# Optimization experiments

Measured on AMD Instinct MI355X. Metric: run time of the kernel, lower is better.

Reference implementation:

```python
import jax, jax.numpy as jnp
import numpy as np
from jax.scipy.linalg import solve_triangular

B, M, S, NBPS = 32768, 16, 8, 4
NUM_ITER = 2
EPS = 1e-4

def _pam_gray(b):
    if len(b) > 1:
        return (1 - 2 * b[0]) * (2 ** len(b[1:]) - _pam_gray(b[1:]))
    return 1 - 2 * b[0]

def _qam(nbps):
    n = 2 ** nbps
    pts = np.zeros(n, np.complex64)
    for i in range(n):
        b = np.array([int(c) for c in np.binary_repr(i, nbps)])
        pts[i] = _pam_gray(b[0::2]) + 1j * _pam_gray(b[1::2])
    pts = pts / np.sqrt(np.mean(np.abs(pts) ** 2))
    labels = ((np.arange(n)[:, None] >> np.arange(nbps - 1, -1, -1)) & 1).astype(np.float32)
    return pts.astype(np.complex64), labels

_PTS_NP, _LAB_NP = _qam(NBPS)
PTS = jnp.asarray(_PTS_NP)                                   # [P] complex64, unit-energy Gray QAM16
PTS_E = jnp.asarray((np.abs(_PTS_NP) ** 2).astype(np.float32))  # [P]
LAB = jnp.asarray(_LAB_NP)                                   # [P, K] bit labels (MSB first)
ASGN = 2.0 * LAB - 1.0                                       # [P, K], +1 where bit==1

def _symbol_logits(llr):
    # LLRs2SymbolLogits: llr=[...,S,K] (llr = log p(b=1)/p(b=0)) -> per-point log-prior [...,S,P]
    return jnp.sum(jax.nn.log_sigmoid(ASGN * llr[..., None, :]), axis=-1)

def _moments(logits):
    # SymbolLogits2Moments: softmax over points -> mean / variance of soft symbols
    p = jax.nn.softmax(logits, axis=-1)                       # [..., S, P]
    mean = jnp.einsum('...p,p->...', p.astype(jnp.complex64), PTS)
    e2 = jnp.einsum('...p,p->...', p, PTS_E)
    var = e2 - (mean.real ** 2 + mean.imag ** 2)
    return mean, var

def _demap(x_hat, llr_a, no_eff):
    # maxlog DemapperWithPrior, LLR = log p(b=1)/p(b=0)
    diff = x_hat[..., None] - PTS                             # [..., S, P]
    d2 = diff.real ** 2 + diff.imag ** 2
    exps = -d2 / no_eff[..., None] + _symbol_logits(llr_a)    # [..., S, P]
    e = exps[..., None]                                       # [..., S, P, 1]
    neg = jnp.float32(-1e30)
    l1 = jnp.max(jnp.where(LAB == 1.0, e, neg), axis=-2)      # [..., S, K]
    l0 = jnp.max(jnp.where(LAB == 0.0, e, neg), axis=-2)
    return l1 - l0

def _forward(y_re, y_im, h_re, h_im, prior, s_re, s_im):
    y = jax.lax.complex(y_re, y_im)                           # [B, M]
    h = jax.lax.complex(h_re, h_im)                           # [B, M, S]
    s = jax.lax.complex(s_re, s_im)                           # [B, M, M] Hermitian PSD
    # whiten_channel: s = L L^H, y <- L^-1 y, h <- L^-1 h
    L = jnp.linalg.cholesky(s)
    y = solve_triangular(L, y[..., None], lower=True)[..., 0]
    h = solve_triangular(L, h, lower=True)
    y_mf = jnp.einsum('bms,bm->bs', jnp.conj(h), y)[..., None]   # [B, S, 1] matched filter
    g = jnp.einsum('bmi,bmj->bij', jnp.conj(h), h)               # [B, S, S] Gram matrix
    # real-valued channel representation [[Re,-Im],[Im,Re]]
    hr = jnp.concatenate([
        jnp.concatenate([h.real, -h.imag], axis=-1),
        jnp.concatenate([h.imag, h.real], axis=-1)], axis=-2)    # [B, 2M, 2S]
    gr = jnp.einsum('bmi,bmj->bij', hr, hr)                      # [B, 2S, 2S]
    eye2s = jnp.eye(2 * S, dtype=jnp.float32)
    llr_d = prior
    llr_a = jnp.zeros_like(prior)
    for _ in range(NUM_ITER):
        llr_a = llr_d
        x_hat, var_x = _moments(_symbol_logits(llr_a))           # [B, S]
        # parallel interference cancellation in matched-filter domain
        y_mf_pic = (y_mf + g * x_hat[..., None, :]
                    - jnp.einsum('bij,bj->bi', g, x_hat)[..., None])  # [B, S, S]
        var2 = jnp.concatenate([var_x, var_x], axis=-1)          # [B, 2S]
        a = gr * var2[..., None, :] + eye2s                      # [B, 2S, 2S]
        a_inv = jnp.linalg.inv(a)
        mu = jnp.sum(a_inv * jnp.swapaxes(gr, -1, -2), axis=-1)  # diag(a_inv @ gr), [B, 2S]
        ypt = jnp.swapaxes(y_mf_pic, -1, -2)                     # [B, S, S] (stream-major)
        ypt_r = jnp.concatenate([ypt.real, ypt.imag], axis=-1)   # [B, S, 2S]
        ypt_r = jnp.concatenate([ypt_r, ypt_r], axis=-2)         # [B, 2S, 2S]
        z = jnp.sum(a_inv * ypt_r, axis=-1) / mu                 # [B, 2S] unbiased estimates
        zr, zi = jnp.split(z, 2, axis=-1)
        x_hat = jax.lax.complex(zr, zi)                          # [B, S]
        rho = mu / jnp.maximum(1.0 - var2 * mu, EPS)             # post-equalization SINR
        rho = jnp.split(rho, 2, axis=-1)[0]                      # [B, S]
        no_eff = 1.0 / rho
        llr_d = _demap(x_hat, llr_a, no_eff)
    return llr_d - llr_a  # extrinsic LLRs [B, S, K]

def setup_inputs() -> dict:
    key = jax.random.key(0)
    k = jax.random.split(key, 7)
    y_re = jax.random.normal(k[0], (B, M), jnp.float32)
    y_im = jax.random.normal(k[1], (B, M), jnp.float32)
    h_re = jax.random.normal(k[2], (B, M, S), jnp.float32) / np.float32(np.sqrt(2.0))
    h_im = jax.random.normal(k[3], (B, M, S), jnp.float32) / np.float32(np.sqrt(2.0))
    prior = 0.5 * jax.random.normal(k[4], (B, S, NBPS), jnp.float32)
    a = jax.lax.complex(jax.random.normal(k[5], (B, M, M), jnp.float32),
                        jax.random.normal(k[6], (B, M, M), jnp.float32)) / np.float32(np.sqrt(2.0 * M))
    s = jnp.einsum('bij,bkj->bik', a, jnp.conj(a)) + 0.5 * jnp.eye(M, dtype=jnp.complex64)
    return {"y_re": y_re, "y_im": y_im, "h_re": h_re, "h_im": h_im,
            "prior": prior, "s_re": s.real, "s_im": s.imag}

def reference(y_re, y_im, h_re, h_im, prior, s_re, s_im):
    return _forward(y_re, y_im, h_re, h_im, prior, s_re, s_im)
```

## Files before the change

### kernel.cpp

```cpp
#include <hip/hip_runtime.h>


#define EPS_F 1e-4f
#define INV_SQRT10 0.31622776601683794f
#define WSYNC() __builtin_amdgcn_wave_barrier()

__device__ __forceinline__ float rcpf(float x) { return __builtin_amdgcn_rcpf(x); }
__device__ __forceinline__ float rsqf(float x) { return __builtin_amdgcn_rsqf(x); }
__device__ __forceinline__ float rdlane(float v, int l) {
    return __uint_as_float(__builtin_amdgcn_readlane(__float_as_uint(v), l));
}
template<int OFF>
__device__ __forceinline__ float swzf(float v) {
    return __uint_as_float(__builtin_amdgcn_ds_swizzle(__float_as_uint(v), OFF));
}
#define SWX1 0x041F
#define SWX2 0x081F
#define SWX4 0x101F

__device__ __forceinline__ float pt_re(int p) {
    return (1.0f - 2.0f * (float)((p >> 3) & 1)) * (1.0f + 2.0f * (float)((p >> 1) & 1)) * INV_SQRT10;
}
__device__ __forceinline__ float pt_im(int p) {
    return (1.0f - 2.0f * (float)((p >> 2) & 1)) * (1.0f + 2.0f * (float)(p & 1)) * INV_SQRT10;
}

__global__ __launch_bounds__(256, 4)
void mmse_pic_kernel(const float* __restrict__ y_re, const float* __restrict__ y_im,
                     const float* __restrict__ h_re, const float* __restrict__ h_im,
                     const float* __restrict__ prior,
                     const float* __restrict__ s_re, const float* __restrict__ s_im,
                     float* __restrict__ out)
{
    const int lane = threadIdx.x & 63;
    const int w    = threadIdx.x >> 6;
    const int b    = blockIdx.x * 4 + w;
    const size_t bs = (size_t)b;

    __shared__ __align__(16) float2 Sc[4][16][28];
    __shared__ float2 xc_[4][8];
    __shared__ float2 ymc_[4][8];
    __shared__ float  vx_[4][8], ne_[4][8];
    __shared__ float  lsig[4][64];
    __shared__ float  logit_[4][8][20];
    __shared__ float  llrD_[4][8][4];

    {
        const float4* pr4 = (const float4*)(s_re + bs * 256);
        const float4* pi4 = (const float4*)(s_im + bs * 256);
        float4 vr = pr4[lane], vi = pi4[lane];
        int r = lane >> 2, c0 = (lane & 3) << 2;
        Sc[w][r][c0+0] = make_float2(vr.x, vi.x);
        Sc[w][r][c0+1] = make_float2(vr.y, vi.y);
        Sc[w][r][c0+2] = make_float2(vr.z, vi.z);
        Sc[w][r][c0+3] = make_float2(vr.w, vi.w);
        if (lane < 32) {
            const float4* hr4 = (const float4*)(h_re + bs * 128);
            const float4* hi4 = (const float4*)(h_im + bs * 128);
            float4 hr = hr4[lane], hi = hi4[lane];
            int row = lane >> 1, col = 16 + ((lane & 1) << 2);
            Sc[w][row][col+0] = make_float2(hr.x, hi.x);
            Sc[w][row][col+1] = make_float2(hr.y, hi.y);
            Sc[w][row][col+2] = make_float2(hr.z, hi.z);
            Sc[w][row][col+3] = make_float2(hr.w, hi.w);
        }
        if (lane < 16) Sc[w][lane][24] = make_float2(y_re[bs*16+lane], y_im[bs*16+lane]);
        if (lane < 32) ((float*)llrD_[w])[lane] = prior[bs*32 + lane];
    }
    WSYNC();

    {
        const int cj = min((lane & 15) << 1, 26);
        const int r4 = lane >> 4;
        float4* rowp[4];
        #pragma unroll
        for (int p = 0; p < 4; ++p)
            rowp[p] = (float4*)&Sc[w][(p << 2) + r4][cj];
        float4* pivp = (float4*)&Sc[w][0][cj];
        #pragma unroll
        for (int k = 0; k < 15; ++k) {
            float invd = rcpf(Sc[w][k][k].x);
            float4 rk = pivp[k * 14];
            const int pmin = (k + 1) >> 2;
            #pragma unroll
            for (int p = 0; p < 4; ++p) {
                if (p < pmin) continue;
                int i = (p << 2) + r4;
                float2 aik = Sc[w][i][k];
                float mr = aik.x * invd, mi = aik.y * invd;
                if (i <= k) { mr = 0.f; mi = 0.f; }
                float4 a = rowp[p][0];
                a.x -= mr*rk.x - mi*rk.y;
                a.y -= mr*rk.y + mi*rk.x;
                a.z -= mr*rk.z - mi*rk.w;
                a.w -= mr*rk.w + mi*rk.z;
                rowp[p][0] = a;
            }
            WSYNC();
        }
    }
    {
        int r2 = lane >> 2, c = lane & 3;
        float irs = rsqf(Sc[w][r2][r2].x);
        float2 v0 = Sc[w][r2][16 + c];
        Sc[w][r2][16 + c] = make_float2(v0.x*irs, v0.y*irs);
        float2 v1 = Sc[w][r2][20 + c];
        Sc[w][r2][20 + c] = make_float2(v1.x*irs, v1.y*irs);
        if (c == 0) {
            float2 v2 = Sc[w][r2][24];
            Sc[w][r2][24] = make_float2(v2.x*irs, v2.y*irs);
        }
    }
    WSYNC();

    const int s = lane >> 3, u = lane & 7;
    float g_re = 0.f, g_im = 0.f, ym_r = 0.f, ym_i = 0.f;
    #pragma unroll
    for (int m = 0; m < 16; ++m) {
        float2 a  = Sc[w][m][16 + s];
        float2 x  = Sc[w][m][16 + u];
        float2 xy = Sc[w][m][24];
        g_re += a.x*x.x + a.y*x.y;
        g_im += a.x*x.y - a.y*x.x;
        ym_r += a.x*xy.x + a.y*xy.y;
        ym_i += a.x*xy.y - a.y*xy.x;
    }
    if (u == 0) ymc_[w][s] = make_float2(ym_r, ym_i);
    WSYNC();

    const float pr = pt_re(u), pi2 = pt_im(u), pe = pr*pr + pi2*pi2;
    float llr_a_reg = 0.f;

    for (int it = 0; it < 2; ++it) {
        {
            int ts = lane >> 3, tk = (lane >> 1) & 3, sg = lane & 1;
            float v = llrD_[w][ts][tk];
            float x = sg ? v : -v;
            lsig[w][lane] = fminf(x, 0.f) - __logf(1.0f + __expf(-fabsf(x)));
        }
        if (lane < 32) llr_a_reg = ((float*)llrD_[w])[lane];
        WSYNC();
        int base = s << 3;
        float lc = lsig[w][base | 2 | ((u >> 2) & 1)]
                 + lsig[w][base | 4 | ((u >> 1) & 1)]
                 + lsig[w][base | 6 | (u & 1)];
        float l0 = lc + lsig[w][base];
        float l1 = lc + lsig[w][base | 1];
        {
            float mx = fmaxf(l0, l1);
            mx = fmaxf(mx, swzf<SWX1>(mx));
            mx = fmaxf(mx, swzf<SWX2>(mx));
            mx = fmaxf(mx, swzf<SWX4>(mx));
            float w0 = __expf(l0 - mx), w1 = __expf(l1 - mx);
            float a = w0 + w1, dw = w0 - w1;
            float se = a, mr = dw * pr, mi = a * pi2, e2 = a * pe;
            se += swzf<SWX1>(se); mr += swzf<SWX1>(mr); mi += swzf<SWX1>(mi); e2 += swzf<SWX1>(e2);
            se += swzf<SWX2>(se); mr += swzf<SWX2>(mr); mi += swzf<SWX2>(mi); e2 += swzf<SWX2>(e2);
            se += swzf<SWX4>(se); mr += swzf<SWX4>(mr); mi += swzf<SWX4>(mi); e2 += swzf<SWX4>(e2);
            if (u == 0) {
                float inv = rcpf(se);
                float mxr = mr*inv, mxi = mi*inv;
                xc_[w][s] = make_float2(mxr, mxi);
                vx_[w][s] = e2*inv - (mxr*mxr + mxi*mxi);
            }
        }
        WSYNC();
        float2 xj = xc_[w][u];
        float vj = vx_[w][u];
        float tr = g_re*xj.x - g_im*xj.y;
        float ti = g_re*xj.y + g_im*xj.x;
        tr += swzf<SWX1>(tr); ti += swzf<SWX1>(ti);
        tr += swzf<SWX2>(tr); ti += swzf<SWX2>(ti);
        tr += swzf<SWX4>(tr); ti += swzf<SWX4>(ti);
        float2 ym = ymc_[w][s];
        float br_ = ym.x - tr, bi_ = ym.y - ti;
        float Ar = g_re*vj + ((s == u) ? 1.f : 0.f);
        float Ai = g_im*vj;
        float Cr = g_re, Ci = g_im;
        #define GJ_STEP(K) { \
            float pvr = rdlane(Ar, (K)*9), pvi = rdlane(Ai, (K)*9); \
            int rowsrc = ((K)<<3)|u; \
            float rAr = __shfl(Ar, rowsrc), rAi = __shfl(Ai, rowsrc); \
            float rCr = __shfl(Cr, rowsrc), rCi = __shfl(Ci, rowsrc); \
            float rbr = __shfl(br_, rowsrc), rbi = __shfl(bi_, rowsrc); \
            float cAr = swzf<(((K)<<5)|0x18)>(Ar), cAi = swzf<(((K)<<5)|0x18)>(Ai); \
            float id2 = rcpf(pvr*pvr + pvi*pvi); \
            float ipr2 = pvr*id2, ipi2 = -pvi*id2; \
            float mr2 = cAr*ipr2 - cAi*ipi2; \
            float mi2 = cAr*ipi2 + cAi*ipr2; \
            if (s == (K)) { mr2 = 0.f; mi2 = 0.f; } \
            Ar  -= mr2*rAr - mi2*rAi;  Ai  -= mr2*rAi + mi2*rAr; \
            Cr  -= mr2*rCr - mi2*rCi;  Ci  -= mr2*rCi + mi2*rCr; \
            br_ -= mr2*rbr - mi2*rbi;  bi_ -= mr2*rbi + mi2*rbr; }
        GJ_STEP(0) GJ_STEP(1) GJ_STEP(2) GJ_STEP(3)
        GJ_STEP(4) GJ_STEP(5) GJ_STEP(6) GJ_STEP(7)
        #undef GJ_STEP
        if (s == u) {
            float id3 = rcpf(Ar*Ar + Ai*Ai);
            float ipr3 = Ar*id3, ipi3 = -Ai*id3;
            float wr = br_*ipr3 - bi_*ipi3;
            float wi = br_*ipi3 + bi_*ipr3;
            float ccr = Cr*ipr3 - Ci*ipi3;
            float cci = Cr*ipi3 + Ci*ipr3;
            float mu = ccr;
            float im = rcpf(mu);
            float zr = (wr + ccr*xj.x - cci*xj.y) * im;
            float zi = (wi + ccr*xj.y + cci*xj.x) * im;
            xc_[w][s] = make_float2(zr, zi);
            ne_[w][s] = fmaxf(1.f - vx_[w][s]*mu, EPS_F) * im;
        }
        WSYNC();
        {
            float2 xh = xc_[w][s];
            float idn = rcpf(ne_[w][s]);
            float dr0 = xh.x - pr, dr1 = xh.x + pr, di = xh.y - pi2;
            logit_[w][s][u]     = l0 - (dr0*dr0 + di*di) * idn;
            logit_[w][s][u + 8] = l1 - (dr1*dr1 + di*di) * idn;
        }
        WSYNC();
        {
            int s2 = lane >> 3, kb = (lane >> 1) & 3, half = lane & 1;
            int bitpos = 3 - kb;
            float m = -1e30f;
            #pragma unroll
            for (int q = 0; q < 8; ++q) {
                int low  = q & ((1 << bitpos) - 1);
                int high = (q >> bitpos) << (bitpos + 1);
                int p = high | (half << bitpos) | low;
                m = fmaxf(m, logit_[w][s2][p]);
            }
            float other = swzf<SWX1>(m);
            if (half == 1) llrD_[w][s2][kb] = m - other;
        }
        WSYNC();
    }

    if (lane < 32) out[bs*32 + lane] = ((float*)llrD_[w])[lane] - llr_a_reg;
}

extern "C" void kernel_launch(void* const* d_in, const int* in_sizes, int n_in,
                              void* d_out, int out_size, void* d_ws, size_t ws_size,
                              hipStream_t stream) {
    const float* y_re  = (const float*)d_in[0];
    const float* y_im  = (const float*)d_in[1];
    const float* h_re  = (const float*)d_in[2];
    const float* h_im  = (const float*)d_in[3];
    const float* prior = (const float*)d_in[4];
    const float* s_re  = (const float*)d_in[5];
    const float* s_im  = (const float*)d_in[6];
    float* out = (float*)d_out;

    const int B = in_sizes[0] / 16;
    mmse_pic_kernel<<<dim3(B / 4), dim3(256), 0, stream>>>(
        y_re, y_im, h_re, h_im, prior, s_re, s_im, out);
}
```

Baseline: 237.5 us.

## Process two batch elements per wavefront with interleaved independent phases

Each wavefront now handles two batch elements (A and B), interleaving their load, Cholesky-style elimination, Gram, moment, Gauss-Jordan solve and demap phases so that independent instruction streams can hide latency of LDS, shuffles and transcendental ops. The grid is halved and shared memory doubled. The elimination step is also rewritten from float4 column chunks to per-lane float2 columns limited to the active region (j>k). This raises register and LDS use per block, which may reduce occupancy under the launch bound of 4 blocks.

```diff
diff --git a/kernel.cpp b/kernel.cpp
--- a/kernel.cpp
+++ b/kernel.cpp
@@ -34,208 +34,247 @@
 {
     const int lane = threadIdx.x & 63;
     const int w    = threadIdx.x >> 6;
-    const int b    = blockIdx.x * 4 + w;
-    const size_t bs = (size_t)b;
-
-    __shared__ __align__(16) float2 Sc[4][16][28];
-    __shared__ float2 xc_[4][8];
-    __shared__ float2 ymc_[4][8];
-    __shared__ float  vx_[4][8], ne_[4][8];
-    __shared__ float  lsig[4][64];
-    __shared__ float  logit_[4][8][20];
-    __shared__ float  llrD_[4][8][4];
+    const int slA  = w << 1, slB = slA | 1;
+    const size_t bsA = (size_t)(blockIdx.x * 8 + slA);
+    const size_t bsB = bsA + 1;
+
+    __shared__ float2 Sc[8][16][28];
+    __shared__ float2 xc_[8][8];
+    __shared__ float2 ymc_[8][8];
+    __shared__ float  vx_[8][8], ne_[8][8];
+    __shared__ float  lsig[8][64];
+    __shared__ float  logit_[8][8][20];
+    __shared__ float  llrD_[8][8][4];
+
+#define LOADPH(X) { \
+        const float4* pr4 = (const float4*)(s_re + bs##X * 256); \
+        const float4* pi4 = (const float4*)(s_im + bs##X * 256); \
+        float4 vr = pr4[lane], vi = pi4[lane]; \
+        int r = lane >> 2, c0 = (lane & 3) << 2; \
+        Sc[sl##X][r][c0+0] = make_float2(vr.x, vi.x); \
+        Sc[sl##X][r][c0+1] = make_float2(vr.y, vi.y); \
+        Sc[sl##X][r][c0+2] = make_float2(vr.z, vi.z); \
+        Sc[sl##X][r][c0+3] = make_float2(vr.w, vi.w); \
+        if (lane < 32) { \
+            const float4* hr4 = (const float4*)(h_re + bs##X * 128); \
+            const float4* hi4 = (const float4*)(h_im + bs##X * 128); \
+            float4 hr = hr4[lane], hi = hi4[lane]; \
+            int row = lane >> 1, col = 16 + ((lane & 1) << 2); \
+            Sc[sl##X][row][col+0] = make_float2(hr.x, hi.x); \
+            Sc[sl##X][row][col+1] = make_float2(hr.y, hi.y); \
+            Sc[sl##X][row][col+2] = make_float2(hr.z, hi.z); \
+            Sc[sl##X][row][col+3] = make_float2(hr.w, hi.w); \
+        } \
+        if (lane < 16) Sc[sl##X][lane][24] = make_float2(y_re[bs##X*16+lane], y_im[bs##X*16+lane]); \
+        if (lane < 32) ((float*)llrD_[sl##X])[lane] = prior[bs##X*32 + lane]; \
+    }
+    LOADPH(A) LOADPH(B)
+#undef LOADPH
+    WSYNC();
 
     {
-        const float4* pr4 = (const float4*)(s_re + bs * 256);
-        const float4* pi4 = (const float4*)(s_im + bs * 256);
-        float4 vr = pr4[lane], vi = pi4[lane];
-        int r = lane >> 2, c0 = (lane & 3) << 2;
-        Sc[w][r][c0+0] = make_float2(vr.x, vi.x);
-        Sc[w][r][c0+1] = make_float2(vr.y, vi.y);
-        Sc[w][r][c0+2] = make_float2(vr.z, vi.z);
-        Sc[w][r][c0+3] = make_float2(vr.w, vi.w);
-        if (lane < 32) {
-            const float4* hr4 = (const float4*)(h_re + bs * 128);
-            const float4* hi4 = (const float4*)(h_im + bs * 128);
-            float4 hr = hr4[lane], hi = hi4[lane];
-            int row = lane >> 1, col = 16 + ((lane & 1) << 2);
-            Sc[w][row][col+0] = make_float2(hr.x, hi.x);
-            Sc[w][row][col+1] = make_float2(hr.y, hi.y);
-            Sc[w][row][col+2] = make_float2(hr.z, hi.z);
-            Sc[w][row][col+3] = make_float2(hr.w, hi.w);
-        }
-        if (lane < 16) Sc[w][lane][24] = make_float2(y_re[bs*16+lane], y_im[bs*16+lane]);
-        if (lane < 32) ((float*)llrD_[w])[lane] = prior[bs*32 + lane];
-    }
-    WSYNC();
-
-    {
-        const int cj = min((lane & 15) << 1, 26);
+        const int j0 = lane & 15;
         const int r4 = lane >> 4;
-        float4* rowp[4];
-        #pragma unroll
-        for (int p = 0; p < 4; ++p)
-            rowp[p] = (float4*)&Sc[w][(p << 2) + r4][cj];
-        float4* pivp = (float4*)&Sc[w][0][cj];
+#define ELIMSTEP(X) { \
+            float invd = rcpf(Sc[sl##X][k][k].x); \
+            int j1 = k + 1 + j0, j2 = j1 + 16; \
+            float2 rk0 = make_float2(0.f, 0.f), rk1 = make_float2(0.f, 0.f); \
+            if (j1 < 25) rk0 = Sc[sl##X][k][j1]; \
+            const bool blk2 = (k < 8); \
+            if (blk2 && j2 < 25) rk1 = Sc[sl##X][k][j2]; \
+            const int pmin = (k + 1) >> 2; \
+            _Pragma("unroll") \
+            for (int p = 0; p < 4; ++p) { \
+                if (p < pmin) continue; \
+                int i = (p << 2) + r4; \
+                float2 aik = Sc[sl##X][i][k]; \
+                float mr = aik.x * invd, mi = aik.y * invd; \
+                if (i <= k) { mr = 0.f; mi = 0.f; } \
+                if (j1 < 25) { \
+                    float2 a = Sc[sl##X][i][j1]; \
+                    a.x -= mr*rk0.x - mi*rk0.y; \
+                    a.y -= mr*rk0.y + mi*rk0.x; \
+                    Sc[sl##X][i][j1] = a; \
+                } \
+                if (blk2 && j2 < 25) { \
+                    float2 a = Sc[sl##X][i][j2]; \
+                    a.x -= mr*rk1.x - mi*rk1.y; \
+                    a.y -= mr*rk1.y + mi*rk1.x; \
+                    Sc[sl##X][i][j2] = a; \
+                } \
+            } }
         #pragma unroll
         for (int k = 0; k < 15; ++k) {
-            float invd = rcpf(Sc[w][k][k].x);
-            float4 rk = pivp[k * 14];
-            const int pmin = (k + 1) >> 2;
-            #pragma unroll
-            for (int p = 0; p < 4; ++p) {
-                if (p < pmin) continue;
-                int i = (p << 2) + r4;
-                float2 aik = Sc[w][i][k];
-                float mr = aik.x * invd, mi = aik.y * invd;
-                if (i <= k) { mr = 0.f; mi = 0.f; }
-                float4 a = rowp[p][0];
-                a.x -= mr*rk.x - mi*rk.y;
-                a.y -= mr*rk.y + mi*rk.x;
-                a.z -= mr*rk.z - mi*rk.w;
-                a.w -= mr*rk.w + mi*rk.z;
-                rowp[p][0] = a;
-            }
+            ELIMSTEP(A)
+            ELIMSTEP(B)
             WSYNC();
         }
+#undef ELIMSTEP
     }
     {
         int r2 = lane >> 2, c = lane & 3;
-        float irs = rsqf(Sc[w][r2][r2].x);
-        float2 v0 = Sc[w][r2][16 + c];
-        Sc[w][r2][16 + c] = make_float2(v0.x*irs, v0.y*irs);
-        float2 v1 = Sc[w][r2][20 + c];
-        Sc[w][r2][20 + c] = make_float2(v1.x*irs, v1.y*irs);
-        if (c == 0) {
-            float2 v2 = Sc[w][r2][24];
-            Sc[w][r2][24] = make_float2(v2.x*irs, v2.y*irs);
-        }
+#define SCALEPH(X) { \
+        float irs = rsqf(Sc[sl##X][r2][r2].x); \
+        float2 v0 = Sc[sl##X][r2][16 + c]; \
+        Sc[sl##X][r2][16 + c] = make_float2(v0.x*irs, v0.y*irs); \
+        float2 v1 = Sc[sl##X][r2][20 + c]; \
+        Sc[sl##X][r2][20 + c] = make_float2(v1.x*irs, v1.y*irs); \
+        if (c == 0) { \
+            float2 v2 = Sc[sl##X][r2][24]; \
+            Sc[sl##X][r2][24] = make_float2(v2.x*irs, v2.y*irs); \
+        } }
+        SCALEPH(A) SCALEPH(B)
+#undef SCALEPH
     }
     WSYNC();
 
     const int s = lane >> 3, u = lane & 7;
-    float g_re = 0.f, g_im = 0.f, ym_r = 0.f, ym_i = 0.f;
-    #pragma unroll
-    for (int m = 0; m < 16; ++m) {
-        float2 a  = Sc[w][m][16 + s];
-        float2 x  = Sc[w][m][16 + u];
-        float2 xy = Sc[w][m][24];
-        g_re += a.x*x.x + a.y*x.y;
-        g_im += a.x*x.y - a.y*x.x;
-        ym_r += a.x*xy.x + a.y*xy.y;
-        ym_i += a.x*xy.y - a.y*xy.x;
-    }
-    if (u == 0) ymc_[w][s] = make_float2(ym_r, ym_i);
+    float g_reA = 0.f, g_imA = 0.f, ym_rA = 0.f, ym_iA = 0.f;
+    float g_reB = 0.f, g_imB = 0.f, ym_rB = 0.f, ym_iB = 0.f;
+#define GRAMPH(X) { \
+    _Pragma("unroll") \
+    for (int m = 0; m < 16; ++m) { \
+        float2 a  = Sc[sl##X][m][16 + s]; \
+        float2 x  = Sc[sl##X][m][16 + u]; \
+        float2 xy = Sc[sl##X][m][24]; \
+        g_re##X += a.x*x.x + a.y*x.y; \
+        g_im##X += a.x*x.y - a.y*x.x; \
+        ym_r##X += a.x*xy.x + a.y*xy.y; \
+        ym_i##X += a.x*xy.y - a.y*xy.x; \
+    } \
+    if (u == 0) ymc_[sl##X][s] = make_float2(ym_r##X, ym_i##X); }
+    GRAMPH(A) GRAMPH(B)
+#undef GRAMPH
     WSYNC();
 
     const float pr = pt_re(u), pi2 = pt_im(u), pe = pr*pr + pi2*pi2;
-    float llr_a_reg = 0.f;
+    float llr_a_regA = 0.f, llr_a_regB = 0.f;
+    float l0A, l1A, l0B, l1B;
 
     for (int it = 0; it < 2; ++it) {
         {
             int ts = lane >> 3, tk = (lane >> 1) & 3, sg = lane & 1;
-            float v = llrD_[w][ts][tk];
-            float x = sg ? v : -v;
-            lsig[w][lane] = fminf(x, 0.f) - __logf(1.0f + __expf(-fabsf(x)));
-        }
-        if (lane < 32) llr_a_reg = ((float*)llrD_[w])[lane];
-        WSYNC();
-        int base = s << 3;
-        float lc = lsig[w][base | 2 | ((u >> 2) & 1)]
-                 + lsig[w][base | 4 | ((u >> 1) & 1)]
-                 + lsig[w][base | 6 | (u & 1)];
-        float l0 = lc + lsig[w][base];
-        float l1 = lc + lsig[w][base | 1];
+#define LSIGPH(X) { \
+            float v = llrD_[sl##X][ts][tk]; \
+            float x = sg ? v : -v; \
+            lsig[sl##X][lane] = fminf(x, 0.f) - __logf(1.0f + __expf(-fabsf(x))); \
+            if (lane < 32) llr_a_reg##X = ((float*)llrD_[sl##X])[lane]; }
+            LSIGPH(A) LSIGPH(B)
+#undef LSIGPH
+        }
+        WSYNC();
         {
-            float mx = fmaxf(l0, l1);
-            mx = fmaxf(mx, swzf<SWX1>(mx));
-            mx = fmaxf(mx, swzf<SWX2>(mx));
-            mx = fmaxf(mx, swzf<SWX4>(mx));
-            float w0 = __expf(l0 - mx), w1 = __expf(l1 - mx);
-            float a = w0 + w1, dw = w0 - w1;
-            float se = a, mr = dw * pr, mi = a * pi2, e2 = a * pe;
-            se += swzf<SWX1>(se); mr += swzf<SWX1>(mr); mi += swzf<SWX1>(mi); e2 += swzf<SWX1>(e2);
-            se += swzf<SWX2>(se); mr += swzf<SWX2>(mr); mi += swzf<SWX2>(mi); e2 += swzf<SWX2>(e2);
-            se += swzf<SWX4>(se); mr += swzf<SWX4>(mr); mi += swzf<SWX4>(mi); e2 += swzf<SWX4>(e2);
-            if (u == 0) {
-                float inv = rcpf(se);
-                float mxr = mr*inv, mxi = mi*inv;
-                xc_[w][s] = make_float2(mxr, mxi);
-                vx_[w][s] = e2*inv - (mxr*mxr + mxi*mxi);
-            }
-        }
-        WSYNC();
-        float2 xj = xc_[w][u];
-        float vj = vx_[w][u];
-        float tr = g_re*xj.x - g_im*xj.y;
-        float ti = g_re*xj.y + g_im*xj.x;
-        tr += swzf<SWX1>(tr); ti += swzf<SWX1>(ti);
-        tr += swzf<SWX2>(tr); ti += swzf<SWX2>(ti);
-        tr += swzf<SWX4>(tr); ti += swzf<SWX4>(ti);
-        float2 ym = ymc_[w][s];
-        float br_ = ym.x - tr, bi_ = ym.y - ti;
-        float Ar = g_re*vj + ((s == u) ? 1.f : 0.f);
-        float Ai = g_im*vj;
-        float Cr = g_re, Ci = g_im;
-        #define GJ_STEP(K) { \
-            float pvr = rdlane(Ar, (K)*9), pvi = rdlane(Ai, (K)*9); \
+            int base = s << 3;
+#define MOMPH(X) { \
+            float lc = lsig[sl##X][base | 2 | ((u >> 2) & 1)] \
+                     + lsig[sl##X][base | 4 | ((u >> 1) & 1)] \
+                     + lsig[sl##X][base | 6 | (u & 1)]; \
+            l0##X = lc + lsig[sl##X][base]; \
+            l1##X = lc + lsig[sl##X][base | 1]; \
+            float mx = fmaxf(l0##X, l1##X); \
+            mx = fmaxf(mx, swzf<SWX1>(mx)); \
+            mx = fmaxf(mx, swzf<SWX2>(mx)); \
+            mx = fmaxf(mx, swzf<SWX4>(mx)); \
+            float w0 = __expf(l0##X - mx), w1 = __expf(l1##X - mx); \
+            float a = w0 + w1, dw = w0 - w1; \
+            float se = a, mr = dw * pr, mi = a * pi2, e2 = a * pe; \
+            se += swzf<SWX1>(se); mr += swzf<SWX1>(mr); mi += swzf<SWX1>(mi); e2 += swzf<SWX1>(e2); \
+            se += swzf<SWX2>(se); mr += swzf<SWX2>(mr); mi += swzf<SWX2>(mi); e2 += swzf<SWX2>(e2); \
+            se += swzf<SWX4>(se); mr += swzf<SWX4>(mr); mi += swzf<SWX4>(mi); e2 += swzf<SWX4>(e2); \
+            if (u == 0) { \
+                float inv = rcpf(se); \
+                float mxr = mr*inv, mxi = mi*inv; \
+                xc_[sl##X][s] = make_float2(mxr, mxi); \
+                vx_[sl##X][s] = e2*inv - (mxr*mxr + mxi*mxi); \
+            } }
+            MOMPH(A) MOMPH(B)
+#undef MOMPH
+        }
+        WSYNC();
+#define GJ_STEP(X, K) { \
+            float pvr = rdlane(Ar##X, (K)*9), pvi = rdlane(Ai##X, (K)*9); \
             int rowsrc = ((K)<<3)|u; \
-            float rAr = __shfl(Ar, rowsrc), rAi = __shfl(Ai, rowsrc); \
-            float rCr = __shfl(Cr, rowsrc), rCi = __shfl(Ci, rowsrc); \
-            float rbr = __shfl(br_, rowsrc), rbi = __shfl(bi_, rowsrc); \
-            float cAr = swzf<(((K)<<5)|0x18)>(Ar), cAi = swzf<(((K)<<5)|0x18)>(Ai); \
+            float rAr = __shfl(Ar##X, rowsrc), rAi = __shfl(Ai##X, rowsrc); \
+            float rCr = __shfl(Cr##X, rowsrc), rCi = __shfl(Ci##X, rowsrc); \
+            float rbr = __shfl(br##X, rowsrc), rbi = __shfl(bi##X, rowsrc); \
+            float cAr = swzf<(((K)<<5)|0x18)>(Ar##X), cAi = swzf<(((K)<<5)|0x18)>(Ai##X); \
             float id2 = rcpf(pvr*pvr + pvi*pvi); \
             float ipr2 = pvr*id2, ipi2 = -pvi*id2; \
             float mr2 = cAr*ipr2 - cAi*ipi2; \
             float mi2 = cAr*ipi2 + cAi*ipr2; \
             if (s == (K)) { mr2 = 0.f; mi2 = 0.f; } \
-            Ar  -= mr2*rAr - mi2*rAi;  Ai  -= mr2*rAi + mi2*rAr; \
-            Cr  -= mr2*rCr - mi2*rCi;  Ci  -= mr2*rCi + mi2*rCr; \
-            br_ -= mr2*rbr - mi2*rbi;  bi_ -= mr2*rbi + mi2*rbr; }
-        GJ_STEP(0) GJ_STEP(1) GJ_STEP(2) GJ_STEP(3)
-        GJ_STEP(4) GJ_STEP(5) GJ_STEP(6) GJ_STEP(7)
-        #undef GJ_STEP
-        if (s == u) {
-            float id3 = rcpf(Ar*Ar + Ai*Ai);
-            float ipr3 = Ar*id3, ipi3 = -Ai*id3;
-            float wr = br_*ipr3 - bi_*ipi3;
-            float wi = br_*ipi3 + bi_*ipr3;
-            float ccr = Cr*ipr3 - Ci*ipi3;
-            float cci = Cr*ipi3 + Ci*ipr3;
-            float mu = ccr;
-            float im = rcpf(mu);
-            float zr = (wr + ccr*xj.x - cci*xj.y) * im;
-            float zi = (wi + ccr*xj.y + cci*xj.x) * im;
-            xc_[w][s] = make_float2(zr, zi);
-            ne_[w][s] = fmaxf(1.f - vx_[w][s]*mu, EPS_F) * im;
-        }
-        WSYNC();
-        {
-            float2 xh = xc_[w][s];
-            float idn = rcpf(ne_[w][s]);
-            float dr0 = xh.x - pr, dr1 = xh.x + pr, di = xh.y - pi2;
-            logit_[w][s][u]     = l0 - (dr0*dr0 + di*di) * idn;
-            logit_[w][s][u + 8] = l1 - (dr1*dr1 + di*di) * idn;
-        }
+            Ar##X -= mr2*rAr - mi2*rAi;  Ai##X -= mr2*rAi + mi2*rAr; \
+            Cr##X -= mr2*rCr - mi2*rCi;  Ci##X -= mr2*rCi + mi2*rCr; \
+            br##X -= mr2*rbr - mi2*rbi;  bi##X -= mr2*rbi + mi2*rbr; }
+#define SOLVEPH(X) \
+        float2 xj##X = xc_[sl##X][u]; \
+        { \
+            float vj = vx_[sl##X][u]; \
+            float tr = g_re##X*xj##X.x - g_im##X*xj##X.y; \
+            float ti = g_re##X*xj##X.y + g_im##X*xj##X.x; \
+            tr += swzf<SWX1>(tr); ti += swzf<SWX1>(ti); \
+            tr += swzf<SWX2>(tr); ti += swzf<SWX2>(ti); \
+            tr += swzf<SWX4>(tr); ti += swzf<SWX4>(ti); \
+            float2 ym = ymc_[sl##X][s]; \
+            float br##X = ym.x - tr, bi##X = ym.y - ti; \
+            float Ar##X = g_re##X*vj + ((s == u) ? 1.f : 0.f); \
+            float Ai##X = g_im##X*vj; \
+            float Cr##X = g_re##X, Ci##X = g_im##X; \
+            GJ_STEP(X,0) GJ_STEP(X,1) GJ_STEP(X,2) GJ_STEP(X,3) \
+            GJ_STEP(X,4) GJ_STEP(X,5) GJ_STEP(X,6) GJ_STEP(X,7) \
+            if (s == u) { \
+                float id3 = rcpf(Ar##X*Ar##X + Ai##X*Ai##X); \
+                float ipr3 = Ar##X*id3, ipi3 = -Ai##X*id3; \
+                float wr = br##X*ipr3 - bi##X*ipi3; \
+                float wi = br##X*ipi3 + bi##X*ipr3; \
+                float ccr = Cr##X*ipr3 - Ci##X*ipi3; \
+                float cci = Cr##X*ipi3 + Ci##X*ipr3; \
+                float mu = ccr; \
+                float im = rcpf(mu); \
+                float zr = (wr + ccr*xj##X.x - cci*xj##X.y) * im; \
+                float zi = (wi + ccr*xj##X.y + cci*xj##X.x) * im; \
+                xc_[sl##X][s] = make_float2(zr, zi); \
+                ne_[sl##X][s] = fmaxf(1.f - vx_[sl##X][s]*mu, EPS_F) * im; \
+            } \
+        }
+        SOLVEPH(A)
+        SOLVEPH(B)
+#undef SOLVEPH
+#undef GJ_STEP
+        WSYNC();
+#define DEMAPPH(X) { \
+            float2 xh = xc_[sl##X][s]; \
+            float idn = rcpf(ne_[sl##X][s]); \
+            float dr0 = xh.x - pr, dr1 = xh.x + pr, di = xh.y - pi2; \
+            logit_[sl##X][s][u]     = l0##X - (dr0*dr0 + di*di) * idn; \
+            logit_[sl##X][s][u + 8] = l1##X - (dr1*dr1 + di*di) * idn; }
+        DEMAPPH(A) DEMAPPH(B)
+#undef DEMAPPH
         WSYNC();
         {
             int s2 = lane >> 3, kb = (lane >> 1) & 3, half = lane & 1;
             int bitpos = 3 - kb;
-            float m = -1e30f;
-            #pragma unroll
-            for (int q = 0; q < 8; ++q) {
-                int low  = q & ((1 << bitpos) - 1);
-                int high = (q >> bitpos) << (bitpos + 1);
-                int p = high | (half << bitpos) | low;
-                m = fmaxf(m, logit_[w][s2][p]);
-            }
-            float other = swzf<SWX1>(m);
-            if (half == 1) llrD_[w][s2][kb] = m - other;
-        }
-        WSYNC();
-    }
-
-    if (lane < 32) out[bs*32 + lane] = ((float*)llrD_[w])[lane] - llr_a_reg;
+#define LLRPH(X) { \
+            float m = -1e30f; \
+            _Pragma("unroll") \
+            for (int q = 0; q < 8; ++q) { \
+                int low  = q & ((1 << bitpos) - 1); \
+                int high = (q >> bitpos) << (bitpos + 1); \
+                int p = high | (half << bitpos) | low; \
+                m = fmaxf(m, logit_[sl##X][s2][p]); \
+            } \
+            float other = swzf<SWX1>(m); \
+            if (half == 1) llrD_[sl##X][s2][kb] = m - other; }
+            LLRPH(A) LLRPH(B)
+#undef LLRPH
+        }
+        WSYNC();
+    }
+
+    if (lane < 32) {
+        out[bsA*32 + lane] = ((float*)llrD_[slA])[lane] - llr_a_regA;
+        out[bsB*32 + lane] = ((float*)llrD_[slB])[lane] - llr_a_regB;
+    }
 }
 
 extern "C" void kernel_launch(void* const* d_in, const int* in_sizes, int n_in,
@@ -251,6 +290,6 @@
     float* out = (float*)d_out;
 
     const int B = in_sizes[0] / 16;
-    mmse_pic_kernel<<<dim3(B / 4), dim3(256), 0, stream>>>(
+    mmse_pic_kernel<<<dim3(B / 8), dim3(256), 0, stream>>>(
         y_re, y_im, h_re, h_im, prior, s_re, s_im, out);
 }
```

New measurement: 359.9 us. +51.5%, slower.
